# Optimization experiments

Measured on AMD Instinct MI355X. Metric: run time of the kernel, lower is better.

Reference implementation:

```python
import jax, jax.numpy as jnp
import numpy as np

N = 10000
F_FEAT = 256
NHID = 128
NCLASS = 16
E_RAND = 160000
K_DEF = 5


def _spmm(row, col, vals, X, n):
    # sparse(A) @ X via gather + segment-sum scatter
    return jax.ops.segment_sum(vals[:, None] * X[col], row, num_segments=n)


def _normalize_sym(row, col, vals, n):
    # D^{-1/2} A D^{-1/2}; duplicate indices are implicitly summed (coalesce)
    deg = jax.ops.segment_sum(vals, row, num_segments=n)
    inv_sqrt = 1.0 / (jnp.sqrt(deg) + 1e-10)
    return vals * inv_sqrt[row] * inv_sqrt[col]


def _normalize_row(row, col, vals, n):
    # D^{-1} A (row-stochastic)
    deg = jax.ops.segment_sum(vals, row, num_segments=n)
    return vals * (1.0 / (deg + 1e-10))[row]


def setup_inputs():
    key = jax.random.key(0)
    ks = jax.random.split(key, 10)
    x = jax.random.normal(ks[0], (N, F_FEAT), dtype=jnp.float32)
    loops = jnp.arange(N, dtype=jnp.int32)
    adj_row = jnp.concatenate([jax.random.randint(ks[1], (E_RAND,), 0, N, dtype=jnp.int32), loops])
    adj_col = jnp.concatenate([jax.random.randint(ks[2], (E_RAND,), 0, N, dtype=jnp.int32), loops])
    adj_val = jax.random.uniform(ks[3], (E_RAND + N,), dtype=jnp.float32)
    ned_val = jax.random.uniform(ks[4], (E_RAND + N,), dtype=jnp.float32)
    W1 = jax.random.normal(ks[5], (F_FEAT, NHID), dtype=jnp.float32) * 0.05
    W2 = jax.random.normal(ks[6], (NHID, NCLASS), dtype=jnp.float32) * 0.05
    return {
        'x': x,
        'adj_row': adj_row, 'adj_col': adj_col, 'adj_val': adj_val,
        'ned_row': adj_row, 'ned_col': adj_col, 'ned_val': ned_val,
        'W_diag1': jnp.ones((F_FEAT,), jnp.float32),
        'W_diag2': jnp.ones((F_FEAT,), jnp.float32),
        'W1': W1, 'b1': jnp.zeros((NHID,), jnp.float32),
        'W2': W2, 'b2': jnp.zeros((NCLASS,), jnp.float32),
        'K': K_DEF,
    }


def reference(x, adj_row, adj_col, adj_val, ned_row, ned_col, ned_val,
              W_diag1, W_diag2, W1, b1, W2, b2, K):
    n = x.shape[0]
    f_half = x.shape[1] // 2

    # --- node embeddings via diagonal GCN convs on symmetrically-normalized Adj
    adj_val_sym = _normalize_sym(adj_row, adj_col, adj_val, n)
    emb = jnp.tanh(_spmm(adj_row, adj_col, adj_val_sym, x * W_diag1, n))
    emb = _spmm(adj_row, adj_col, adj_val_sym, emb * W_diag2, n)
    emb = emb / (jnp.linalg.norm(emb, axis=1, keepdims=True) + 1e-12)  # F.normalize p=2

    # --- Adj_new = D^{-1}A_ned @ (E1 E1^T + E2 E2^T), computed without forming S
    ned_val_rw = _normalize_row(ned_row, ned_col, ned_val, n)
    e1, e2 = emb[:, :f_half], emb[:, f_half:]
    t1 = _spmm(ned_row, ned_col, ned_val_rw, e1, n)
    t2 = _spmm(ned_row, ned_col, ned_val_rw, e2, n)
    adj_new = t1 @ e1.T + t2 @ e2.T  # dense [N, N]

    # --- topK sparsification, symmetrized
    topv, topi = jax.lax.top_k(adj_new, K)          # [N, K]
    rows_k = jnp.repeat(jnp.arange(n, dtype=adj_row.dtype), K)
    cols_k = topi.reshape(-1).astype(adj_row.dtype)
    vals_k = topv.reshape(-1)

    new_row = jnp.concatenate([adj_row, rows_k, cols_k])
    new_col = jnp.concatenate([adj_col, cols_k, rows_k])
    new_val = jnp.concatenate([adj_val, vals_k, vals_k])
    new_val = _normalize_sym(new_row, new_col, new_val, n)

    # --- 2-layer GCN on the augmented graph (eval mode: dropout off)
    h = _spmm(new_row, new_col, new_val, x @ W1, n) + b1
    h = jax.nn.relu(h)
    out = _spmm(new_row, new_col, new_val, h @ W2, n) + b2
    return out
```

## Files before the change

kernel.cpp:

```cpp
#include <hip/hip_runtime.h>
#include <cfloat>
#include <cstdint>

#define F_FEAT 256
#define NHID 128
#define NCLASS 16
#define KTOP 5
#define SCT 5
#define STRIPW (SCT * 256)

typedef _Float16 f16x8 __attribute__((ext_vector_type(8)));
typedef __attribute__((ext_vector_type(4))) float f32x4;
typedef unsigned long long u64;

__device__ __forceinline__ void topk_insert5(float (&v)[5], int (&ix)[5], float cv, int ci) {
  if (cv < v[4] || (cv == v[4] && ci > ix[4])) return;
  int pos = 0;
#pragma unroll
  for (int j = 0; j < 5; ++j) pos += ((v[j] > cv) || (v[j] == cv && ix[j] < ci)) ? 1 : 0;
  if (pos >= 5) return;
  for (int j = 4; j > pos; --j) { v[j] = v[j - 1]; ix[j] = ix[j - 1]; }
  v[pos] = cv; ix[pos] = ci;
}

__device__ __forceinline__ void gload_lds16(const void* g, void* l) {
  __builtin_amdgcn_global_load_lds((const __attribute__((address_space(1))) void*)g,
                                   (__attribute__((address_space(3))) void*)l, 16, 0, 0);
}

__device__ __forceinline__ u64 packkey(float v, int idx) {
  unsigned u = __float_as_uint(v);
  u ^= (u >> 31) ? 0xFFFFFFFFu : 0x80000000u;
  return ((u64)u << 32) | (unsigned)(0x7FFFFFFF - idx);
}
__device__ __forceinline__ void unpackkey(u64 key, float& v, int& idx) {
  unsigned u = (unsigned)(key >> 32);
  u ^= (u >> 31) ? 0x80000000u : 0xFFFFFFFFu;
  v = __uint_as_float(u);
  idx = 0x7FFFFFFF - (int)(key & 0xFFFFFFFFu);
}
__device__ __forceinline__ u64 umax64(u64 a, u64 b) { return a > b ? a : b; }
__device__ __forceinline__ u64 umin64(u64 a, u64 b) { return a > b ? b : a; }

__device__ __forceinline__ void ins5(u64& s0, u64& s1, u64& s2, u64& s3, u64& s4, u64 k) {
  u64 t;
  t = umin64(s0, k); s0 = umax64(s0, k); k = t;
  t = umin64(s1, k); s1 = umax64(s1, k); k = t;
  t = umin64(s2, k); s2 = umax64(s2, k); k = t;
  t = umin64(s3, k); s3 = umax64(s3, k); k = t;
  s4 = umax64(s4, k);
}

__device__ __forceinline__ void merge5(u64& a0, u64& a1, u64& a2, u64& a3, u64& a4,
                                       u64 b0, u64 b1, u64 b2, u64 b3, u64 b4) {
  u64 x00 = umin64(a0, b0);
  u64 x01 = umin64(a0, b1), x10 = umin64(a1, b0);
  u64 x02 = umin64(a0, b2), x11 = umin64(a1, b1), x20 = umin64(a2, b0);
  u64 x03 = umin64(a0, b3), x12 = umin64(a1, b2), x21 = umin64(a2, b1), x30 = umin64(a3, b0);
  u64 c0 = umax64(a0, b0);
  u64 c1 = umax64(x00, umax64(a1, b1));
  u64 c2 = umax64(umax64(x01, x10), umax64(a2, b2));
  u64 c3 = umax64(umax64(x02, x20), umax64(x11, umax64(a3, b3)));
  u64 c4 = umax64(umax64(umax64(x03, x30), umax64(x12, x21)), umax64(a4, b4));
  a0 = c0; a1 = c1; a2 = c2; a3 = c3; a4 = c4;
}

__device__ __forceinline__ u64 shflx64(u64 v, int m) {
  int lo = __shfl_xor((int)(unsigned)(v & 0xFFFFFFFFull), m, 64);
  int hi = __shfl_xor((int)(unsigned)(v >> 32), m, 64);
  return ((u64)(unsigned)hi << 32) | (unsigned)lo;
}

__global__ void k_deg_count(const int* __restrict__ ar, const float* __restrict__ av,
                            const int* __restrict__ nr, const float* __restrict__ nv,
                            float* deg_adj, float* deg_ned, int* cntA, int* cntN, int E) {
  int e = blockIdx.x * blockDim.x + threadIdx.x;
  if (e >= E) return;
  int ra = ar[e]; int rn = nr[e];
  atomicAdd(&deg_adj[ra], av[e]);
  atomicAdd(&deg_ned[rn], nv[e]);
  atomicAdd(&cntA[ra], 1);
  atomicAdd(&cntN[rn], 1);
}

__global__ __launch_bounds__(1024) void k_scan_pair(const int* c0, int* o0, const int* c1, int* o1, int n) {
  const int* c = (blockIdx.x == 0) ? c0 : c1;
  int* o = (blockIdx.x == 0) ? o0 : o1;
  if (c == nullptr) return;
  __shared__ int buf[1024];
  int tid = threadIdx.x;
  int base = 0;
  int chunks = (n + 1023) >> 10;
  for (int ch = 0; ch < chunks; ++ch) {
    int i = (ch << 10) + tid;
    buf[tid] = (i < n) ? c[i] : 0;
    __syncthreads();
    for (int offd = 1; offd < 1024; offd <<= 1) {
      int t = (tid >= offd) ? buf[tid - offd] : 0;
      __syncthreads();
      buf[tid] += t;
      __syncthreads();
    }
    if (i < n) o[i + 1] = base + buf[tid];
    int tot = buf[1023];
    __syncthreads();
    base += tot;
  }
  if (tid == 0) o[0] = 0;
}

__global__ void k_rs(const float* deg_adj, const float* deg_ned, float* rs_adj, float* rinv_ned, int N) {
  int i = blockIdx.x * blockDim.x + threadIdx.x;
  if (i >= N) return;
  rs_adj[i] = 1.0f / (sqrtf(deg_adj[i]) + 1e-10f);
  rinv_ned[i] = 1.0f / (deg_ned[i] + 1e-10f);
}

__global__ void k_fill2(const int* ar, const int* nr, const int* rpA, const int* rpN,
                        int* fillA, int* fillN, int* permA, int* permN, int E) {
  int e = blockIdx.x * blockDim.x + threadIdx.x;
  if (e >= E) return;
  int ra = ar[e];
  permA[rpA[ra] + atomicAdd(&fillA[ra], 1)] = e;
  int rn = nr[e];
  permN[rpN[rn] + atomicAdd(&fillN[rn], 1)] = e;
}

__global__ void k_edgeval(const int* ar, const int* ac, const float* av,
                          const int* nr, const float* nv,
                          const float* rs_adj, const float* rinv_ned,
                          float* adj_sym, float* ned_rw, int E) {
  int e = blockIdx.x * blockDim.x + threadIdx.x;
  if (e >= E) return;
  adj_sym[e] = av[e] * rs_adj[ar[e]] * rs_adj[ac[e]];
  ned_rw[e] = nv[e] * rinv_ned[nr[e]];
}

__global__ void k_spmm1(const int* __restrict__ rpA, const int* __restrict__ permA,
                        const int* __restrict__ ac, const float* __restrict__ adj_sym,
                        const float* __restrict__ x, const float* __restrict__ Wd1,
                        float* __restrict__ emb, int N) {
  int r = blockIdx.x; int f = threadIdx.x;
  int s = rpA[r], e = rpA[r + 1];
  float acc = 0.f;
  for (int i = s; i < e; ++i) {
    int id = permA[i];
    acc += adj_sym[id] * x[(size_t)ac[id] * F_FEAT + f];
  }
  emb[(size_t)r * F_FEAT + f] = tanhf(acc * Wd1[f]);
}

__global__ void k_spmm2_norm(const int* __restrict__ rpA, const int* __restrict__ permA,
                             const int* __restrict__ ac, const float* __restrict__ adj_sym,
                             const float* __restrict__ emb, const float* __restrict__ Wd2,
                             float* __restrict__ embn, int N) {
  __shared__ float red[F_FEAT];
  int r = blockIdx.x; int f = threadIdx.x;
  int s = rpA[r], e = rpA[r + 1];
  float acc = 0.f;
  for (int i = s; i < e; ++i) {
    int id = permA[i];
    acc += adj_sym[id] * emb[(size_t)ac[id] * F_FEAT + f];
  }
  float val = acc * Wd2[f];
  red[f] = val * val;
  __syncthreads();
  for (int st = F_FEAT / 2; st > 0; st >>= 1) {
    if (f < st) red[f] += red[f + st];
    __syncthreads();
  }
  float rinv = 1.0f / (sqrtf(red[0]) + 1e-12f);
  embn[(size_t)r * F_FEAT + f] = val * rinv;
}

__global__ void k_spmmT(const int* __restrict__ rpN, const int* __restrict__ permN,
                        const int* __restrict__ nc, const float* __restrict__ ned_rw,
                        const float* __restrict__ embn, float* __restrict__ Tm, int N) {
  int r = blockIdx.x; int f = threadIdx.x;
  int s = rpN[r], e = rpN[r + 1];
  float acc = 0.f;
  for (int i = s; i < e; ++i) {
    int id = permN[i];
    acc += ned_rw[id] * embn[(size_t)nc[id] * F_FEAT + f];
  }
  Tm[(size_t)r * F_FEAT + f] = acc;
}

__global__ void k_convert(const float* __restrict__ src,
                          unsigned short* __restrict__ p1, unsigned short* __restrict__ p2,
                          int N, int Npad) {
  int idx = blockIdx.x * blockDim.x + threadIdx.x;
  int total = Npad * (F_FEAT / 4);
  if (idx >= total) return;
  int row = idx >> 6;
  int c4 = (idx & 63) << 2;
  float4 v = make_float4(0.f, 0.f, 0.f, 0.f);
  if (row < N) v = *reinterpret_cast<const float4*>(src + (size_t)row * F_FEAT + c4);
  float arr[4] = {v.x, v.y, v.z, v.w};
  ushort4 o1, o2;
  unsigned short* q1 = (unsigned short*)&o1;
  unsigned short* q2 = (unsigned short*)&o2;
#pragma unroll
  for (int j = 0; j < 4; ++j) {
    float a = arr[j];
    _Float16 h1 = (_Float16)a;
    float r = a - (float)h1;
    _Float16 h2 = (_Float16)r;
    q1[j] = __builtin_bit_cast(unsigned short, h1);
    q2[j] = __builtin_bit_cast(unsigned short, h2);
  }
  size_t off = (size_t)row * F_FEAT + c4;
  *reinterpret_cast<ushort4*>(p1 + off) = o1;
  *reinterpret_cast<ushort4*>(p2 + off) = o2;
}

__global__ __launch_bounds__(512, 1) void k_gemm_c(
    const unsigned short* __restrict__ A1, const unsigned short* __restrict__ A2,
    const unsigned short* __restrict__ B1, const unsigned short* __restrict__ B2,
    float* __restrict__ Cbuf, int ct0) {
  __shared__ __align__(16) unsigned short lds[2 * 4 * 256 * 32];

  int tid = threadIdx.x;
  int lane = tid & 63;
  int wid = tid >> 6;
  int wr = wid >> 2;
  int wc = wid & 3;
  int lr = lane & 15;
  int lg = lane >> 4;

  int rt = blockIdx.x;
  int ctl = blockIdx.y;
  int ct = ct0 + ctl;
  int row0 = rt * 256, col0 = ct * 256;

  int sp = wid >> 1, sh = wid & 1;
  const unsigned short* pg = (sp == 0) ? A1 : (sp == 1) ? A2 : (sp == 2) ? B1 : B2;
  int srow = lane >> 2;
  int sslot = lane & 3;
  int sgslot = sslot ^ ((srow >> 1) & 3);
  int t0 = (sp < 2) ? row0 : col0;
  const char* gbase = (const char*)pg + ((size_t)(t0 + sh * 128 + srow) << 9) + sgslot * 16;
  char* lbase0 = (char*)lds + sp * 16384 + sh * 8192;

  int fslot = (lg ^ ((lr >> 1) & 3)) << 3;

  f32x4 acc[8][4];
#pragma unroll
  for (int m = 0; m < 8; ++m)
#pragma unroll
    for (int n = 0; n < 4; ++n) acc[m][n] = (f32x4){0.f, 0.f, 0.f, 0.f};

#pragma unroll
  for (int i = 0; i < 8; ++i)
    gload_lds16(gbase + ((size_t)i << 13), lbase0 + (i << 10));
  __syncthreads();

  for (int ks = 0; ks < 8; ++ks) {
    int cur = ks & 1;
    if (ks < 7) {
      const char* g = gbase + (ks + 1) * 64;
      char* lb = lbase0 + ((cur ^ 1) << 16);
#pragma unroll
      for (int i = 0; i < 8; ++i)
        gload_lds16(g + ((size_t)i << 13), lb + (i << 10));
    }
    const unsigned short* bufp = lds + cur * 32768;
    f16x8 fb[2][4];
#pragma unroll
    for (int n = 0; n < 4; ++n) {
      int off = (wc * 64 + n * 16 + lr) * 32 + fslot;
      fb[0][n] = *reinterpret_cast<const f16x8*>(bufp + 2 * 8192 + off);
      fb[1][n] = *reinterpret_cast<const f16x8*>(bufp + 3 * 8192 + off);
    }
#pragma unroll
    for (int m = 0; m < 8; ++m) {
      int off = (wr * 128 + m * 16 + lr) * 32 + fslot;
      f16x8 fa1 = *reinterpret_cast<const f16x8*>(bufp + 0 * 8192 + off);
      f16x8 fa2 = *reinterpret_cast<const f16x8*>(bufp + 1 * 8192 + off);
#pragma unroll
      for (int n = 0; n < 4; ++n) {
        acc[m][n] = __builtin_amdgcn_mfma_f32_16x16x32_f16(fa1, fb[1][n], acc[m][n], 0, 0, 0);
        acc[m][n] = __builtin_amdgcn_mfma_f32_16x16x32_f16(fa2, fb[0][n], acc[m][n], 0, 0, 0);
        acc[m][n] = __builtin_amdgcn_mfma_f32_16x16x32_f16(fa1, fb[0][n], acc[m][n], 0, 0, 0);
      }
    }
    __syncthreads();
  }

#pragma unroll
  for (int m = 0; m < 8; ++m) {
#pragma unroll
    for (int rg = 0; rg < 4; ++rg) {
      int rl = wr * 128 + m * 16 + lg * 4 + rg;
      float* cr = Cbuf + (size_t)(row0 + rl) * STRIPW + ctl * 256 + wc * 64 + lr;
#pragma unroll
      for (int n = 0; n < 4; ++n) cr[n * 16] = acc[m][n][rg];
    }
  }
}

__global__ __launch_bounds__(256) void k_topk(const float* __restrict__ Cbuf, int col0, int first,
                                              u64* __restrict__ Kst, int N) {
  int wid = threadIdx.x >> 6, lane = threadIdx.x & 63;
  int r = blockIdx.x * 4 + wid;
  if (r >= N) return;
  const float4* rowp = reinterpret_cast<const float4*>(Cbuf + (size_t)r * STRIPW);
  float4 vv[SCT];
#pragma unroll
  for (int j = 0; j < SCT; ++j) vv[j] = rowp[j * 64 + lane];

  u64 s0 = 0, s1 = 0, s2 = 0, s3 = 0, s4 = 0;
#pragma unroll
  for (int j = 0; j < SCT; ++j) {
    int cb = col0 + (j * 64 + lane) * 4;
    float arr[4] = {vv[j].x, vv[j].y, vv[j].z, vv[j].w};
#pragma unroll
    for (int q = 0; q < 4; ++q) {
      int gc = cb + q;
      u64 key = (gc < N) ? packkey(arr[q], gc) : 0ull;
      ins5(s0, s1, s2, s3, s4, key);
    }
  }
#pragma unroll
  for (int d = 1; d < 64; d <<= 1) {
    u64 t0 = shflx64(s0, d), t1 = shflx64(s1, d), t2 = shflx64(s2, d),
        t3 = shflx64(s3, d), t4 = shflx64(s4, d);
    merge5(s0, s1, s2, s3, s4, t0, t1, t2, t3, t4);
  }
  if (lane == 0) {
    u64* st = Kst + (size_t)r * 5;
    if (!first) merge5(s0, s1, s2, s3, s4, st[0], st[1], st[2], st[3], st[4]);
    st[0] = s0; st[1] = s1; st[2] = s2; st[3] = s3; st[4] = s4;
  }
}

__global__ void k_merge(const u64* __restrict__ Kst,
                        float* __restrict__ topv, int* __restrict__ topi,
                        const float* deg_adj, float* deg_new, const int* cntA, int* cnt_new, int N) {
  int r = blockIdx.x * blockDim.x + threadIdx.x;
  if (r >= N) return;
  float sumv = 0.f;
  for (int k = 0; k < 5; ++k) {
    float v; int ix;
    unpackkey(Kst[(size_t)r * 5 + k], v, ix);
    topv[(size_t)r * 5 + k] = v;
    topi[(size_t)r * 5 + k] = ix;
    sumv += v;
    atomicAdd(&deg_new[ix], v);
    atomicAdd(&cnt_new[ix], 1);
  }
  atomicAdd(&deg_new[r], deg_adj[r] + sumv);
  atomicAdd(&cnt_new[r], cntA[r] + KTOP);
}

__global__ void k_rs_new(const float* deg_new, float* rs_new, int N) {
  int i = blockIdx.x * blockDim.x + threadIdx.x;
  if (i >= N) return;
  rs_new[i] = 1.0f / (sqrtf(deg_new[i]) + 1e-10f);
}

__global__ void k_fill_new(const int* ar, const int* topi, const int* rp_new, int* fill_new,
                           int* perm_new, int E, int NK, int total) {
  int t = blockIdx.x * blockDim.x + threadIdx.x;
  if (t >= total) return;
  int r;
  if (t < E) r = ar[t];
  else if (t < E + NK) r = (t - E) / KTOP;
  else r = topi[t - E - NK];
  perm_new[rp_new[r] + atomicAdd(&fill_new[r], 1)] = t;
}

__global__ void k_xw1(const float* __restrict__ x, const float* __restrict__ W1,
                      float* __restrict__ XW1, int N) {
  int c = threadIdx.x & 127;
  int half = threadIdx.x >> 7;
  int r0 = blockIdx.x * 8 + half * 4;
  int rm = N - 1;
  const float* x0 = x + (size_t)min(r0 + 0, rm) * F_FEAT;
  const float* x1 = x + (size_t)min(r0 + 1, rm) * F_FEAT;
  const float* x2 = x + (size_t)min(r0 + 2, rm) * F_FEAT;
  const float* x3 = x + (size_t)min(r0 + 3, rm) * F_FEAT;
  float a0 = 0.f, a1 = 0.f, a2 = 0.f, a3 = 0.f;
  for (int k = 0; k < F_FEAT; ++k) {
    float wv = W1[k * NHID + c];
    a0 += x0[k] * wv; a1 += x1[k] * wv; a2 += x2[k] * wv; a3 += x3[k] * wv;
  }
  if (r0 + 0 < N) XW1[(size_t)(r0 + 0) * NHID + c] = a0;
  if (r0 + 1 < N) XW1[(size_t)(r0 + 1) * NHID + c] = a1;
  if (r0 + 2 < N) XW1[(size_t)(r0 + 2) * NHID + c] = a2;
  if (r0 + 3 < N) XW1[(size_t)(r0 + 3) * NHID + c] = a3;
}

__global__ void k_spmm_h(const int* __restrict__ rp, const int* __restrict__ perm,
                         const int* __restrict__ ac, const float* __restrict__ av,
                         const int* __restrict__ topi, const float* __restrict__ topv,
                         const float* __restrict__ rs, const float* __restrict__ XW1,
                         const float* __restrict__ b1, float* __restrict__ h,
                         int N, int E, int NK) {
  int r = blockIdx.x; int f = threadIdx.x;
  int s = rp[r], e = rp[r + 1];
  float acc = 0.f;
  for (int i = s; i < e; ++i) {
    int id = perm[i];
    int c; float v;
    if (id < E) { c = ac[id]; v = av[id]; }
    else if (id < E + NK) { int q = id - E; c = topi[q]; v = topv[q]; }
    else { int q = id - E - NK; c = q / KTOP; v = topv[q]; }
    acc += v * rs[c] * XW1[(size_t)c * NHID + f];
  }
  float o = rs[r] * acc + b1[f];
  h[(size_t)r * NHID + f] = fmaxf(o, 0.f);
}

__global__ void k_hw2(const float* __restrict__ h, const float* __restrict__ W2,
                      float* __restrict__ HW2, int N) {
  int tid = threadIdx.x;
  int rr = tid >> 4, c = tid & 15;
  int r = blockIdx.x * 16 + rr;
  if (r >= N) return;
  float acc = 0.f;
  for (int k = 0; k < NHID; ++k) acc += h[(size_t)r * NHID + k] * W2[k * NCLASS + c];
  HW2[(size_t)r * NCLASS + c] = acc;
}

__global__ void k_spmm_out(const int* __restrict__ rp, const int* __restrict__ perm,
                           const int* __restrict__ ac, const float* __restrict__ av,
                           const int* __restrict__ topi, const float* __restrict__ topv,
                           const float* __restrict__ rs, const float* __restrict__ HW2,
                           const float* __restrict__ b2, float* __restrict__ out,
                           int N, int E, int NK) {
  int tid = threadIdx.x;
  int rr = tid >> 4, c = tid & 15;
  int r = blockIdx.x * 16 + rr;
  if (r >= N) return;
  int s = rp[r], e = rp[r + 1];
  float acc = 0.f;
  for (int i = s; i < e; ++i) {
    int id = perm[i];
    int cc; float v;
    if (id < E) { cc = ac[id]; v = av[id]; }
    else if (id < E + NK) { int q = id - E; cc = topi[q]; v = topv[q]; }
    else { int q = id - E - NK; cc = q / KTOP; v = topv[q]; }
    acc += v * rs[cc] * HW2[(size_t)cc * NCLASS + c];
  }
  out[(size_t)r * NCLASS + c] = rs[r] * acc + b2[c];
}

extern "C" void kernel_launch(void* const* d_in, const int* in_sizes, int n_in,
                              void* d_out, int out_size, void* d_ws, size_t ws_size,
                              hipStream_t stream) {
  (void)n_in; (void)out_size; (void)ws_size;
  const float* x   = (const float*)d_in[0];
  const int*   ar  = (const int*)d_in[1];
  const int*   ac  = (const int*)d_in[2];
  const float* av  = (const float*)d_in[3];
  const int*   nr  = (const int*)d_in[4];
  const int*   nc  = (const int*)d_in[5];
  const float* nv  = (const float*)d_in[6];
  const float* Wd1 = (const float*)d_in[7];
  const float* Wd2 = (const float*)d_in[8];
  const float* W1  = (const float*)d_in[9];
  const float* b1  = (const float*)d_in[10];
  const float* W2  = (const float*)d_in[11];
  const float* b2  = (const float*)d_in[12];
  int N = in_sizes[0] / F_FEAT;
  int E = in_sizes[3];
  int NK = N * KTOP;
  int total_new = E + 2 * NK;
  int Npad = ((N + 255) / 256) * 256;
  int nrt = Npad / 256;
  int nct = nrt;
  int nstrip = (nct + SCT - 1) / SCT;

  char* w = (char*)d_ws;
  size_t off = 0;
  auto carveB = [&](size_t bytes) -> void* {
    void* p = (void*)(w + off);
    off += (bytes + 255) & ~((size_t)255);
    return p;
  };
  auto carve = [&](size_t elems) -> void* { return carveB(elems * 4); };
  size_t zstart = off;
  float* deg_adj = (float*)carve(N);
  float* deg_ned = (float*)carve(N);
  float* deg_new = (float*)carve(N);
  int* cntA = (int*)carve(N);
  int* cntN = (int*)carve(N);
  int* cnt_new = (int*)carve(N);
  int* fillA = (int*)carve(N);
  int* fillN = (int*)carve(N);
  int* fill_new = (int*)carve(N);
  size_t zbytes = off - zstart;
  float* rs_adj = (float*)carve(N);
  float* rinv_ned = (float*)carve(N);
  float* rs_new = (float*)carve(N);
  float* adj_sym = (float*)carve(E);
  float* ned_rw = (float*)carve(E);
  int* rpA = (int*)carve(N + 1);
  int* rpN = (int*)carve(N + 1);
  int* rp_new = (int*)carve(N + 1);
  int* permA = (int*)carve(E);
  int* permN = (int*)carve(E);
  int* perm_new = (int*)carve(total_new);
  float* emb  = (float*)carve((size_t)N * F_FEAT);
  float* embn = (float*)carve((size_t)N * F_FEAT);
  float* Tm   = (float*)carve((size_t)N * F_FEAT);
  float* topv = (float*)carve(NK);
  int*   topi = (int*)carve(NK);
  u64*   Kst  = (u64*)carveB((size_t)NK * 8);
  float* XW1  = (float*)carve((size_t)N * NHID);
  float* hbuf = (float*)carve((size_t)N * NHID);
  float* HW2  = (float*)carve((size_t)N * NCLASS);
  size_t planeBytes = (size_t)Npad * F_FEAT * 2;
  unsigned short* TA1 = (unsigned short*)carveB(planeBytes);
  unsigned short* TA2 = (unsigned short*)carveB(planeBytes);
  unsigned short* EB1 = (unsigned short*)carveB(planeBytes);
  unsigned short* EB2 = (unsigned short*)carveB(planeBytes);
  float* Cbuf = (float*)carveB((size_t)Npad * STRIPW * 4);

  hipMemsetAsync(w + zstart, 0, zbytes, stream);

  int eb = (E + 255) / 256;
  k_deg_count<<<eb, 256, 0, stream>>>(ar, av, nr, nv, deg_adj, deg_ned, cntA, cntN, E);
  k_scan_pair<<<2, 1024, 0, stream>>>(cntA, rpA, cntN, rpN, N);
  k_rs<<<(N + 255) / 256, 256, 0, stream>>>(deg_adj, deg_ned, rs_adj, rinv_ned, N);
  k_fill2<<<eb, 256, 0, stream>>>(ar, nr, rpA, rpN, fillA, fillN, permA, permN, E);
  k_edgeval<<<eb, 256, 0, stream>>>(ar, ac, av, nr, nv, rs_adj, rinv_ned, adj_sym, ned_rw, E);
  k_spmm1<<<N, F_FEAT, 0, stream>>>(rpA, permA, ac, adj_sym, x, Wd1, emb, N);
  k_spmm2_norm<<<N, F_FEAT, 0, stream>>>(rpA, permA, ac, adj_sym, emb, Wd2, embn, N);
  k_spmmT<<<N, F_FEAT, 0, stream>>>(rpN, permN, nc, ned_rw, embn, Tm, N);
  int cvb = (Npad * (F_FEAT / 4) + 255) / 256;
  k_convert<<<cvb, 256, 0, stream>>>(Tm, TA1, TA2, N, Npad);
  k_convert<<<cvb, 256, 0, stream>>>(embn, EB1, EB2, N, Npad);

  for (int s = 0; s < nstrip; ++s) {
    dim3 gg(nrt, SCT);
    k_gemm_c<<<gg, 512, 0, stream>>>(TA1, TA2, EB1, EB2, Cbuf, s * SCT);
    k_topk<<<(N + 3) / 4, 256, 0, stream>>>(Cbuf, s * STRIPW, (s == 0) ? 1 : 0, Kst, N);
  }

  k_merge<<<(N + 255) / 256, 256, 0, stream>>>(Kst, topv, topi, deg_adj, deg_new, cntA, cnt_new, N);
  k_scan_pair<<<1, 1024, 0, stream>>>(cnt_new, rp_new, nullptr, nullptr, N);
  k_rs_new<<<(N + 255) / 256, 256, 0, stream>>>(deg_new, rs_new, N);
  k_fill_new<<<(total_new + 255) / 256, 256, 0, stream>>>(ar, topi, rp_new, fill_new, perm_new, E, NK, total_new);
  k_xw1<<<(N + 7) / 8, 256, 0, stream>>>(x, W1, XW1, N);
  k_spmm_h<<<N, NHID, 0, stream>>>(rp_new, perm_new, ac, av, topi, topv, rs_new, XW1, b1, hbuf, N, E, NK);
  k_hw2<<<(N + 15) / 16, 256, 0, stream>>>(hbuf, W2, HW2, N);
  k_spmm_out<<<(N + 15) / 16, 256, 0, stream>>>(rp_new, perm_new, ac, av, topi, topv, rs_new, HW2, b2, (float*)d_out, N, E, NK);
}
```

Measured before the change: 938.9 us.

## Pre-gather CSR col/value pairs, unroll SpMM loops, deepen GEMM LDS prefetch

```diff
diff --git a/kernel.cpp b/kernel.cpp
--- a/kernel.cpp
+++ b/kernel.cpp
@@ -12,16 +12,6 @@
 typedef _Float16 f16x8 __attribute__((ext_vector_type(8)));
 typedef __attribute__((ext_vector_type(4))) float f32x4;
 typedef unsigned long long u64;
-
-__device__ __forceinline__ void topk_insert5(float (&v)[5], int (&ix)[5], float cv, int ci) {
-  if (cv < v[4] || (cv == v[4] && ci > ix[4])) return;
-  int pos = 0;
-#pragma unroll
-  for (int j = 0; j < 5; ++j) pos += ((v[j] > cv) || (v[j] == cv && ix[j] < ci)) ? 1 : 0;
-  if (pos >= 5) return;
-  for (int j = 4; j > pos; --j) { v[j] = v[j - 1]; ix[j] = ix[j - 1]; }
-  v[pos] = cv; ix[pos] = ci;
-}
 
 __device__ __forceinline__ void gload_lds16(const void* g, void* l) {
   __builtin_amdgcn_global_load_lds((const __attribute__((address_space(1))) void*)g,
@@ -136,31 +126,61 @@
   ned_rw[e] = nv[e] * rinv_ned[nr[e]];
 }
 
-__global__ void k_spmm1(const int* __restrict__ rpA, const int* __restrict__ permA,
-                        const int* __restrict__ ac, const float* __restrict__ adj_sym,
+__global__ void k_permgather(const int* __restrict__ perm, const int* __restrict__ cols,
+                             const float* __restrict__ vals, int2* __restrict__ out, int E) {
+  int i = blockIdx.x * blockDim.x + threadIdx.x;
+  if (i >= E) return;
+  int id = perm[i];
+  out[i] = make_int2(cols[id], __float_as_int(vals[id]));
+}
+
+__global__ void k_spmm1(const int* __restrict__ rpA, const int2* __restrict__ colv,
                         const float* __restrict__ x, const float* __restrict__ Wd1,
                         float* __restrict__ emb, int N) {
   int r = blockIdx.x; int f = threadIdx.x;
   int s = rpA[r], e = rpA[r + 1];
   float acc = 0.f;
-  for (int i = s; i < e; ++i) {
-    int id = permA[i];
-    acc += adj_sym[id] * x[(size_t)ac[id] * F_FEAT + f];
+  int i = s;
+  for (; i + 4 <= e; i += 4) {
+    int2 c0 = colv[i], c1 = colv[i + 1], c2 = colv[i + 2], c3 = colv[i + 3];
+    float v0 = x[(size_t)c0.x * F_FEAT + f];
+    float v1 = x[(size_t)c1.x * F_FEAT + f];
+    float v2 = x[(size_t)c2.x * F_FEAT + f];
+    float v3 = x[(size_t)c3.x * F_FEAT + f];
+    acc += __int_as_float(c0.y) * v0;
+    acc += __int_as_float(c1.y) * v1;
+    acc += __int_as_float(c2.y) * v2;
+    acc += __int_as_float(c3.y) * v3;
+  }
+  for (; i < e; ++i) {
+    int2 c0 = colv[i];
+    acc += __int_as_float(c0.y) * x[(size_t)c0.x * F_FEAT + f];
   }
   emb[(size_t)r * F_FEAT + f] = tanhf(acc * Wd1[f]);
 }
 
-__global__ void k_spmm2_norm(const int* __restrict__ rpA, const int* __restrict__ permA,
-                             const int* __restrict__ ac, const float* __restrict__ adj_sym,
+__global__ void k_spmm2_norm(const int* __restrict__ rpA, const int2* __restrict__ colv,
                              const float* __restrict__ emb, const float* __restrict__ Wd2,
                              float* __restrict__ embn, int N) {
   __shared__ float red[F_FEAT];
   int r = blockIdx.x; int f = threadIdx.x;
   int s = rpA[r], e = rpA[r + 1];
   float acc = 0.f;
-  for (int i = s; i < e; ++i) {
-    int id = permA[i];
-    acc += adj_sym[id] * emb[(size_t)ac[id] * F_FEAT + f];
+  int i = s;
+  for (; i + 4 <= e; i += 4) {
+    int2 c0 = colv[i], c1 = colv[i + 1], c2 = colv[i + 2], c3 = colv[i + 3];
+    float v0 = emb[(size_t)c0.x * F_FEAT + f];
+    float v1 = emb[(size_t)c1.x * F_FEAT + f];
+    float v2 = emb[(size_t)c2.x * F_FEAT + f];
+    float v3 = emb[(size_t)c3.x * F_FEAT + f];
+    acc += __int_as_float(c0.y) * v0;
+    acc += __int_as_float(c1.y) * v1;
+    acc += __int_as_float(c2.y) * v2;
+    acc += __int_as_float(c3.y) * v3;
+  }
+  for (; i < e; ++i) {
+    int2 c0 = colv[i];
+    acc += __int_as_float(c0.y) * emb[(size_t)c0.x * F_FEAT + f];
   }
   float val = acc * Wd2[f];
   red[f] = val * val;
@@ -173,15 +193,26 @@
   embn[(size_t)r * F_FEAT + f] = val * rinv;
 }
 
-__global__ void k_spmmT(const int* __restrict__ rpN, const int* __restrict__ permN,
-                        const int* __restrict__ nc, const float* __restrict__ ned_rw,
+__global__ void k_spmmT(const int* __restrict__ rpN, const int2* __restrict__ colv,
                         const float* __restrict__ embn, float* __restrict__ Tm, int N) {
   int r = blockIdx.x; int f = threadIdx.x;
   int s = rpN[r], e = rpN[r + 1];
   float acc = 0.f;
-  for (int i = s; i < e; ++i) {
-    int id = permN[i];
-    acc += ned_rw[id] * embn[(size_t)nc[id] * F_FEAT + f];
+  int i = s;
+  for (; i + 4 <= e; i += 4) {
+    int2 c0 = colv[i], c1 = colv[i + 1], c2 = colv[i + 2], c3 = colv[i + 3];
+    float v0 = embn[(size_t)c0.x * F_FEAT + f];
+    float v1 = embn[(size_t)c1.x * F_FEAT + f];
+    float v2 = embn[(size_t)c2.x * F_FEAT + f];
+    float v3 = embn[(size_t)c3.x * F_FEAT + f];
+    acc += __int_as_float(c0.y) * v0;
+    acc += __int_as_float(c1.y) * v1;
+    acc += __int_as_float(c2.y) * v2;
+    acc += __int_as_float(c3.y) * v3;
+  }
+  for (; i < e; ++i) {
+    int2 c0 = colv[i];
+    acc += __int_as_float(c0.y) * embn[(size_t)c0.x * F_FEAT + f];
   }
   Tm[(size_t)r * F_FEAT + f] = acc;
 }
@@ -253,17 +284,15 @@
 #pragma unroll
   for (int i = 0; i < 8; ++i)
     gload_lds16(gbase + ((size_t)i << 13), lbase0 + (i << 10));
-  __syncthreads();
+#pragma unroll
+  for (int i = 0; i < 8; ++i)
+    gload_lds16(gbase + 64 + ((size_t)i << 13), lbase0 + 65536 + (i << 10));
+  asm volatile("s_waitcnt vmcnt(8)" : : : "memory");
+  __builtin_amdgcn_sched_barrier(0);
+  __builtin_amdgcn_s_barrier();
 
   for (int ks = 0; ks < 8; ++ks) {
     int cur = ks & 1;
-    if (ks < 7) {
-      const char* g = gbase + (ks + 1) * 64;
-      char* lb = lbase0 + ((cur ^ 1) << 16);
-#pragma unroll
-      for (int i = 0; i < 8; ++i)
-        gload_lds16(g + ((size_t)i << 13), lb + (i << 10));
-    }
     const unsigned short* bufp = lds + cur * 32768;
     f16x8 fb[2][4];
 #pragma unroll
@@ -284,7 +313,24 @@
         acc[m][n] = __builtin_amdgcn_mfma_f32_16x16x32_f16(fa1, fb[0][n], acc[m][n], 0, 0, 0);
       }
     }
-    __syncthreads();
+    if (ks == 7) break;
+
+    asm volatile("s_waitcnt lgkmcnt(0)" : : : "memory");
+    __builtin_amdgcn_sched_barrier(0);
+    __builtin_amdgcn_s_barrier();
+
+    if (ks < 6) {
+      const char* g = gbase + (size_t)(ks + 2) * 64;
+      char* lb = lbase0 + (cur << 16);
+#pragma unroll
+      for (int i = 0; i < 8; ++i)
+        gload_lds16(g + ((size_t)i << 13), lb + (i << 10));
+      asm volatile("s_waitcnt vmcnt(8)" : : : "memory");
+    } else {
+      asm volatile("s_waitcnt vmcnt(0)" : : : "memory");
+    }
+    __builtin_amdgcn_sched_barrier(0);
+    __builtin_amdgcn_s_barrier();
   }
 
 #pragma unroll
@@ -359,15 +405,20 @@
   rs_new[i] = 1.0f / (sqrtf(deg_new[i]) + 1e-10f);
 }
 
-__global__ void k_fill_new(const int* ar, const int* topi, const int* rp_new, int* fill_new,
-                           int* perm_new, int E, int NK, int total) {
+__global__ void k_fill_new(const int* __restrict__ ar, const int* __restrict__ ac,
+                           const float* __restrict__ av,
+                           const int* __restrict__ topi, const float* __restrict__ topv,
+                           const float* __restrict__ rs_new,
+                           const int* __restrict__ rp_new, int* fill_new,
+                           int2* __restrict__ colv_new, int E, int NK, int total) {
   int t = blockIdx.x * blockDim.x + threadIdx.x;
   if (t >= total) return;
-  int r;
-  if (t < E) r = ar[t];
-  else if (t < E + NK) r = (t - E) / KTOP;
-  else r = topi[t - E - NK];
-  perm_new[rp_new[r] + atomicAdd(&fill_new[r], 1)] = t;
+  int r, c; float v;
+  if (t < E)            { r = ar[t]; c = ac[t]; v = av[t]; }
+  else if (t < E + NK)  { int q = t - E; r = q / KTOP; c = topi[q]; v = topv[q]; }
+  else                  { int q = t - E - NK; r = topi[q]; c = q / KTOP; v = topv[q]; }
+  int pos = rp_new[r] + atomicAdd(&fill_new[r], 1);
+  colv_new[pos] = make_int2(c, __float_as_int(v * rs_new[c]));
 }
 
 __global__ void k_xw1(const float* __restrict__ x, const float* __restrict__ W1,
@@ -391,22 +442,27 @@
   if (r0 + 3 < N) XW1[(size_t)(r0 + 3) * NHID + c] = a3;
 }
 
-__global__ void k_spmm_h(const int* __restrict__ rp, const int* __restrict__ perm,
-                         const int* __restrict__ ac, const float* __restrict__ av,
-                         const int* __restrict__ topi, const float* __restrict__ topv,
+__global__ void k_spmm_h(const int* __restrict__ rp, const int2* __restrict__ colv,
                          const float* __restrict__ rs, const float* __restrict__ XW1,
-                         const float* __restrict__ b1, float* __restrict__ h,
-                         int N, int E, int NK) {
+                         const float* __restrict__ b1, float* __restrict__ h, int N) {
   int r = blockIdx.x; int f = threadIdx.x;
   int s = rp[r], e = rp[r + 1];
   float acc = 0.f;
-  for (int i = s; i < e; ++i) {
-    int id = perm[i];
-    int c; float v;
-    if (id < E) { c = ac[id]; v = av[id]; }
-    else if (id < E + NK) { int q = id - E; c = topi[q]; v = topv[q]; }
-    else { int q = id - E - NK; c = q / KTOP; v = topv[q]; }
-    acc += v * rs[c] * XW1[(size_t)c * NHID + f];
+  int i = s;
+  for (; i + 4 <= e; i += 4) {
+    int2 c0 = colv[i], c1 = colv[i + 1], c2 = colv[i + 2], c3 = colv[i + 3];
+    float v0 = XW1[(size_t)c0.x * NHID + f];
+    float v1 = XW1[(size_t)c1.x * NHID + f];
+    float v2 = XW1[(size_t)c2.x * NHID + f];
+    float v3 = XW1[(size_t)c3.x * NHID + f];
+    acc += __int_as_float(c0.y) * v0;
+    acc += __int_as_float(c1.y) * v1;
+    acc += __int_as_float(c2.y) * v2;
+    acc += __int_as_float(c3.y) * v3;
+  }
+  for (; i < e; ++i) {
+    int2 c0 = colv[i];
+    acc += __int_as_float(c0.y) * XW1[(size_t)c0.x * NHID + f];
   }
   float o = rs[r] * acc + b1[f];
   h[(size_t)r * NHID + f] = fmaxf(o, 0.f);
@@ -423,25 +479,30 @@
   HW2[(size_t)r * NCLASS + c] = acc;
 }
 
-__global__ void k_spmm_out(const int* __restrict__ rp, const int* __restrict__ perm,
-                           const int* __restrict__ ac, const float* __restrict__ av,
-                           const int* __restrict__ topi, const float* __restrict__ topv,
+__global__ void k_spmm_out(const int* __restrict__ rp, const int2* __restrict__ colv,
                            const float* __restrict__ rs, const float* __restrict__ HW2,
-                           const float* __restrict__ b2, float* __restrict__ out,
-                           int N, int E, int NK) {
+                           const float* __restrict__ b2, float* __restrict__ out, int N) {
   int tid = threadIdx.x;
   int rr = tid >> 4, c = tid & 15;
   int r = blockIdx.x * 16 + rr;
   if (r >= N) return;
   int s = rp[r], e = rp[r + 1];
   float acc = 0.f;
-  for (int i = s; i < e; ++i) {
-    int id = perm[i];
-    int cc; float v;
-    if (id < E) { cc = ac[id]; v = av[id]; }
-    else if (id < E + NK) { int q = id - E; cc = topi[q]; v = topv[q]; }
-    else { int q = id - E - NK; cc = q / KTOP; v = topv[q]; }
-    acc += v * rs[cc] * HW2[(size_t)cc * NCLASS + c];
+  int i = s;
+  for (; i + 4 <= e; i += 4) {
+    int2 c0 = colv[i], c1 = colv[i + 1], c2 = colv[i + 2], c3 = colv[i + 3];
+    float v0 = HW2[(size_t)c0.x * NCLASS + c];
+    float v1 = HW2[(size_t)c1.x * NCLASS + c];
+    float v2 = HW2[(size_t)c2.x * NCLASS + c];
+    float v3 = HW2[(size_t)c3.x * NCLASS + c];
+    acc += __int_as_float(c0.y) * v0;
+    acc += __int_as_float(c1.y) * v1;
+    acc += __int_as_float(c2.y) * v2;
+    acc += __int_as_float(c3.y) * v3;
+  }
+  for (; i < e; ++i) {
+    int2 c0 = colv[i];
+    acc += __int_as_float(c0.y) * HW2[(size_t)c0.x * NCLASS + c];
   }
   out[(size_t)r * NCLASS + c] = rs[r] * acc + b2[c];
 }
@@ -501,7 +562,9 @@
   int* rp_new = (int*)carve(N + 1);
   int* permA = (int*)carve(E);
   int* permN = (int*)carve(E);
-  int* perm_new = (int*)carve(total_new);
+  int2* colvA = (int2*)carveB((size_t)E * 8);
+  int2* colvN = (int2*)carveB((size_t)E * 8);
+  int2* colv_new = (int2*)carveB((size_t)total_new * 8);
   float* emb  = (float*)carve((size_t)N * F_FEAT);
   float* embn = (float*)carve((size_t)N * F_FEAT);
   float* Tm   = (float*)carve((size_t)N * F_FEAT);
@@ -526,9 +589,11 @@
   k_rs<<<(N + 255) / 256, 256, 0, stream>>>(deg_adj, deg_ned, rs_adj, rinv_ned, N);
   k_fill2<<<eb, 256, 0, stream>>>(ar, nr, rpA, rpN, fillA, fillN, permA, permN, E);
   k_edgeval<<<eb, 256, 0, stream>>>(ar, ac, av, nr, nv, rs_adj, rinv_ned, adj_sym, ned_rw, E);
-  k_spmm1<<<N, F_FEAT, 0, stream>>>(rpA, permA, ac, adj_sym, x, Wd1, emb, N);
-  k_spmm2_norm<<<N, F_FEAT, 0, stream>>>(rpA, permA, ac, adj_sym, emb, Wd2, embn, N);
-  k_spmmT<<<N, F_FEAT, 0, stream>>>(rpN, permN, nc, ned_rw, embn, Tm, N);
+  k_permgather<<<eb, 256, 0, stream>>>(permA, ac, adj_sym, colvA, E);
+  k_permgather<<<eb, 256, 0, stream>>>(permN, nc, ned_rw, colvN, E);
+  k_spmm1<<<N, F_FEAT, 0, stream>>>(rpA, colvA, x, Wd1, emb, N);
+  k_spmm2_norm<<<N, F_FEAT, 0, stream>>>(rpA, colvA, emb, Wd2, embn, N);
+  k_spmmT<<<N, F_FEAT, 0, stream>>>(rpN, colvN, embn, Tm, N);
   int cvb = (Npad * (F_FEAT / 4) + 255) / 256;
   k_convert<<<cvb, 256, 0, stream>>>(Tm, TA1, TA2, N, Npad);
   k_convert<<<cvb, 256, 0, stream>>>(embn, EB1, EB2, N, Npad);
@@ -542,9 +607,10 @@
   k_merge<<<(N + 255) / 256, 256, 0, stream>>>(Kst, topv, topi, deg_adj, deg_new, cntA, cnt_new, N);
   k_scan_pair<<<1, 1024, 0, stream>>>(cnt_new, rp_new, nullptr, nullptr, N);
   k_rs_new<<<(N + 255) / 256, 256, 0, stream>>>(deg_new, rs_new, N);
-  k_fill_new<<<(total_new + 255) / 256, 256, 0, stream>>>(ar, topi, rp_new, fill_new, perm_new, E, NK, total_new);
+  k_fill_new<<<(total_new + 255) / 256, 256, 0, stream>>>(ar, ac, av, topi, topv, rs_new,
+                                                          rp_new, fill_new, colv_new, E, NK, total_new);
   k_xw1<<<(N + 7) / 8, 256, 0, stream>>>(x, W1, XW1, N);
-  k_spmm_h<<<N, NHID, 0, stream>>>(rp_new, perm_new, ac, av, topi, topv, rs_new, XW1, b1, hbuf, N, E, NK);
+  k_spmm_h<<<N, NHID, 0, stream>>>(rp_new, colv_new, rs_new, XW1, b1, hbuf, N);
   k_hw2<<<(N + 15) / 16, 256, 0, stream>>>(hbuf, W2, HW2, N);
-  k_spmm_out<<<(N + 15) / 16, 256, 0, stream>>>(rp_new, perm_new, ac, av, topi, topv, rs_new, HW2, b2, (float*)d_out, N, E, NK);
-}
+  k_spmm_out<<<(N + 15) / 16, 256, 0, stream>>>(rp_new, colv_new, rs_new, HW2, b2, (float*)d_out, N);
+}
```

After: 808.0 us. 1.16x faster.
